# Kernel tuning notes

Hardware: AMD Instinct MI355X
Metric: run time of the kernel (lower is better)

Reference implementation:

```python
import jax, jax.numpy as jnp
import numpy as np

B, N, E, H = 64, 2048, 256, 256


def _scan_dir(xproj, Whh, bhh, reverse):
    # xproj: (B, N, H) precomputed input projection; recurrence h_t = tanh(xproj_t + h @ Whh.T + bhh)
    def step(h, xt):
        h = jnp.tanh(xt + h @ Whh.T + bhh)
        return h, h
    h0 = jnp.zeros((xproj.shape[0], Whh.shape[0]), xproj.dtype)
    _, seq = jax.lax.scan(step, h0, jnp.swapaxes(xproj, 0, 1), reverse=reverse)
    return jnp.swapaxes(seq, 0, 1)  # (B, N, H)


def _bilayer(inp, Wf, bf, Uf, cf, Wb, bb, Ub, cb):
    fore = _scan_dir(inp @ Wf.T + bf, Uf, cf, False)
    back = _scan_dir(inp @ Wb.T + bb, Ub, cb, True)
    return jnp.concatenate([fore, back], axis=-1), fore[:, -1, :], back[:, 0, :]


def setup_inputs() -> dict:
    key = jax.random.key(0)
    ks = jax.random.split(key, 17)
    s_e = 1.0 / np.sqrt(E)
    s_h = 1.0 / np.sqrt(H)
    s_2h = 1.0 / np.sqrt(2 * H)
    f32 = jnp.float32
    return {
        'x': jax.random.normal(ks[0], (B, N, E), f32),
        'Wih_f0': jax.random.normal(ks[1], (H, E), f32) * s_e,
        'bih_f0': jax.random.normal(ks[2], (H,), f32) * s_e,
        'Whh_f0': jax.random.normal(ks[3], (H, H), f32) * s_h,
        'bhh_f0': jax.random.normal(ks[4], (H,), f32) * s_h,
        'Wih_b0': jax.random.normal(ks[5], (H, E), f32) * s_e,
        'bih_b0': jax.random.normal(ks[6], (H,), f32) * s_e,
        'Whh_b0': jax.random.normal(ks[7], (H, H), f32) * s_h,
        'bhh_b0': jax.random.normal(ks[8], (H,), f32) * s_h,
        'Wih_f1': jax.random.normal(ks[9], (H, 2 * H), f32) * s_2h,
        'bih_f1': jax.random.normal(ks[10], (H,), f32) * s_2h,
        'Whh_f1': jax.random.normal(ks[11], (H, H), f32) * s_h,
        'bhh_f1': jax.random.normal(ks[12], (H,), f32) * s_h,
        'Wih_b1': jax.random.normal(ks[13], (H, 2 * H), f32) * s_2h,
        'bih_b1': jax.random.normal(ks[14], (H,), f32) * s_2h,
        'Whh_b1': jax.random.normal(ks[15], (H, H), f32) * s_h,
        'bhh_b1': jax.random.normal(ks[16], (H,), f32) * s_h,
    }


def reference(x, Wih_f0, bih_f0, Whh_f0, bhh_f0, Wih_b0, bih_b0, Whh_b0, bhh_b0,
              Wih_f1, bih_f1, Whh_f1, bhh_f1, Wih_b1, bih_b1, Whh_b1, bhh_b1):
    out0, _, _ = _bilayer(x, Wih_f0, bih_f0, Whh_f0, bhh_f0, Wih_b0, bih_b0, Whh_b0, bhh_b0)
    _, h_f, h_b = _bilayer(out0, Wih_f1, bih_f1, Whh_f1, bhh_f1, Wih_b1, bih_b1, Whh_b1, bhh_b1)
    return jnp.concatenate([h_f, h_b], axis=-1)  # (B, 2H) final hidden of last layer
```

## Files before the change

kernel.cpp:

```cpp
#include <hip/hip_runtime.h>

#define BATCH 64
#define SEQ   2048
#define EIN   256
#define HID   256

typedef _Float16 f16;
typedef _Float16 f16x8 __attribute__((ext_vector_type(8)));
typedef float    f32x4 __attribute__((ext_vector_type(4)));

__global__ __launch_bounds__(256) void cast_f32_f16(
    const float* __restrict__ s, f16* __restrict__ d, int n)
{
    int i = (blockIdx.x * 256 + threadIdx.x) * 8;
    if (i >= n) return;
    const float4* sp = reinterpret_cast<const float4*>(s + i);
    float4 a = sp[0], b = sp[1];
    f16x8 v = { (f16)a.x, (f16)a.y, (f16)a.z, (f16)a.w,
                (f16)b.x, (f16)b.y, (f16)b.z, (f16)b.w };
    *reinterpret_cast<f16x8*>(d + i) = v;
}

__global__ __launch_bounds__(256, 2) void gemm_proj(
    const f16* __restrict__ A, const f16* __restrict__ W,
    const float* __restrict__ bias, f16* __restrict__ C, int K)
{
    const int tid  = threadIdx.x;
    const int wave = tid >> 6, lane = tid & 63;
    const int g    = lane >> 4, lr = lane & 15;
    const int bm   = blockIdx.x * 128;
    const int bn   = blockIdx.y * 128;
    const int wm   = (wave >> 1) * 64, wn = (wave & 1) * 64;

    __shared__ __align__(16) f16 As[128][72];
    __shared__ __align__(16) f16 Bs[128][72];

    f32x4 acc[4][4] = {};

    for (int kt = 0; kt < K; kt += 64) {
        __syncthreads();
#pragma unroll
        for (int i = 0; i < 4; ++i) {
            int c = i * 256 + tid;
            int r = c >> 3, sg = c & 7;
            *reinterpret_cast<f16x8*>(&As[r][sg * 8]) =
                *reinterpret_cast<const f16x8*>(A + (size_t)(bm + r) * K + kt + sg * 8);
            *reinterpret_cast<f16x8*>(&Bs[r][sg * 8]) =
                *reinterpret_cast<const f16x8*>(W + (size_t)(bn + r) * K + kt + sg * 8);
        }
        __syncthreads();
#pragma unroll
        for (int kf = 0; kf < 2; ++kf) {
            f16x8 af[4], bf[4];
#pragma unroll
            for (int f = 0; f < 4; ++f) {
                af[f] = *reinterpret_cast<const f16x8*>(&As[wm + f * 16 + lr][kf * 32 + g * 8]);
                bf[f] = *reinterpret_cast<const f16x8*>(&Bs[wn + f * 16 + lr][kf * 32 + g * 8]);
            }
#pragma unroll
            for (int fm = 0; fm < 4; ++fm)
#pragma unroll
                for (int fn = 0; fn < 4; ++fn)
                    acc[fm][fn] = __builtin_amdgcn_mfma_f32_16x16x32_f16(
                        af[fm], bf[fn], acc[fm][fn], 0, 0, 0);
        }
    }

#pragma unroll
    for (int fn = 0; fn < 4; ++fn) {
        float bv = bias[bn + wn + fn * 16 + lr];
#pragma unroll
        for (int fm = 0; fm < 4; ++fm) {
#pragma unroll
            for (int i = 0; i < 4; ++i) {
                int row = bm + wm + fm * 16 + g * 4 + i;
                int col = bn + wn + fn * 16 + lr;
                C[(size_t)row * 256 + col] = (f16)(acc[fm][fn][i] + bv);
            }
        }
    }
}

template<bool WRITE_SEQ>
__global__ __launch_bounds__(256, 1) void rnn_scan(
    const f16* __restrict__ xpF, const f16* __restrict__ xpB,
    const float* __restrict__ WhhF, const float* __restrict__ bhhF,
    const float* __restrict__ WhhB, const float* __restrict__ bhhB,
    f16* __restrict__ seq_out,
    float* __restrict__ fin_out)
{
    const int blk = blockIdx.x;
    const int b   = blk >> 1, dir = blk & 1;
    const f16*   xp  = dir ? xpB : xpF;
    const float* Whh = dir ? WhhB : WhhF;
    const float* bhh = dir ? bhhB : bhhF;

    const int tid  = threadIdx.x;
    const int wave = tid >> 6, lane = tid & 63;
    const int g    = lane >> 4, lr = lane & 15;
    const int n0   = wave * 64;

    __shared__ __align__(16) f16 hbuf[2][256];

    f16x8 wf[4][8];
#pragma unroll
    for (int fn = 0; fn < 4; ++fn) {
        const float* wr = Whh + (size_t)(n0 + fn * 16 + lr) * 256;
#pragma unroll
        for (int kf = 0; kf < 8; ++kf) {
            const float4* p = reinterpret_cast<const float4*>(wr + kf * 32 + g * 8);
            float4 x0 = p[0], x1 = p[1];
            wf[fn][kf] = (f16x8){ (f16)x0.x, (f16)x0.y, (f16)x0.z, (f16)x0.w,
                                  (f16)x1.x, (f16)x1.y, (f16)x1.z, (f16)x1.w };
        }
    }
    const float bv = bhh[tid];

    hbuf[0][tid] = (f16)0.f;
    __syncthreads();

    const long long xstep = dir ? -256 : 256;
    const f16* xptr = xp + (long long)b * SEQ * 256 + (long long)(dir ? SEQ - 1 : 0) * 256 + tid;

    const long long sstep = dir ? -512 : 512;
    f16* sptr = nullptr;
    if (WRITE_SEQ)
        sptr = seq_out + ((long long)b * SEQ + (dir ? SEQ - 1 : 0)) * 512 + dir * 256 + tid;

    f16 ring[4];
#pragma unroll
    for (int r = 0; r < 3; ++r) ring[r] = xptr[(long long)r * xstep];
    const f16* xpre = xptr + 3 * xstep;

    const f32x4 zf = {0.f, 0.f, 0.f, 0.f};
    float last_h = 0.f;

    for (int s4 = 0; s4 < SEQ; s4 += 4) {
#pragma unroll
        for (int u = 0; u < 4; ++u) {
            const int rd = u & 1;

            f16x8 af[8];
#pragma unroll
            for (int kf = 0; kf < 8; ++kf)
                af[kf] = *reinterpret_cast<const f16x8*>(&hbuf[rd][kf * 32 + g * 8]);

            ring[(u + 3) & 3] = *xpre;
            xpre += xstep;

            f32x4 alo[4], ahi[4];
#pragma unroll
            for (int fn = 0; fn < 4; ++fn) {
                alo[fn] = __builtin_amdgcn_mfma_f32_16x16x32_f16(af[0], wf[fn][0], zf, 0, 0, 0);
                ahi[fn] = __builtin_amdgcn_mfma_f32_16x16x32_f16(af[4], wf[fn][4], zf, 0, 0, 0);
            }
#pragma unroll
            for (int kf = 1; kf < 4; ++kf)
#pragma unroll
                for (int fn = 0; fn < 4; ++fn) {
                    alo[fn] = __builtin_amdgcn_mfma_f32_16x16x32_f16(af[kf],     wf[fn][kf],     alo[fn], 0, 0, 0);
                    ahi[fn] = __builtin_amdgcn_mfma_f32_16x16x32_f16(af[kf + 4], wf[fn][kf + 4], ahi[fn], 0, 0, 0);
                }

            float lo01 = (g & 1) ? alo[1][0] : alo[0][0];
            float lo23 = (g & 1) ? alo[3][0] : alo[2][0];
            float lo   = (g & 2) ? lo23 : lo01;
            float hi01 = (g & 1) ? ahi[1][0] : ahi[0][0];
            float hi23 = (g & 1) ? ahi[3][0] : ahi[2][0];
            float hi   = (g & 2) ? hi23 : hi01;

            float pre = lo + hi + (float)ring[u & 3] + bv;
            float e  = __expf(pre + pre);
            float h  = 1.0f - 2.0f * __builtin_amdgcn_rcpf(e + 1.0f);
            f16 hh   = (f16)h;
            last_h   = h;

            hbuf[rd ^ 1][tid] = hh;

            if (WRITE_SEQ) {
                *sptr = hh;
                sptr += sstep;
            }

            asm volatile("s_waitcnt lgkmcnt(0)" ::: "memory");
            __builtin_amdgcn_s_barrier();
            asm volatile("" ::: "memory");
        }
    }

    if (!WRITE_SEQ)
        fin_out[b * 512 + dir * 256 + tid] = last_h;
}

extern "C" void kernel_launch(void* const* d_in, const int* in_sizes, int n_in,
                              void* d_out, int out_size, void* d_ws, size_t ws_size,
                              hipStream_t stream)
{
    (void)in_sizes; (void)n_in; (void)out_size; (void)ws_size;

    const float* x      = (const float*)d_in[0];
    const float* Wih_f0 = (const float*)d_in[1];
    const float* bih_f0 = (const float*)d_in[2];
    const float* Whh_f0 = (const float*)d_in[3];
    const float* bhh_f0 = (const float*)d_in[4];
    const float* Wih_b0 = (const float*)d_in[5];
    const float* bih_b0 = (const float*)d_in[6];
    const float* Whh_b0 = (const float*)d_in[7];
    const float* bhh_b0 = (const float*)d_in[8];
    const float* Wih_f1 = (const float*)d_in[9];
    const float* bih_f1 = (const float*)d_in[10];
    const float* Whh_f1 = (const float*)d_in[11];
    const float* bhh_f1 = (const float*)d_in[12];
    const float* Wih_b1 = (const float*)d_in[13];
    const float* bih_b1 = (const float*)d_in[14];
    const float* Whh_b1 = (const float*)d_in[15];
    const float* bhh_b1 = (const float*)d_in[16];

    float* out = (float*)d_out;
    char*  ws  = (char*)d_ws;

    f16* xpF  = (f16*)(ws);
    f16* xpB  = (f16*)(ws + 67108864);
    f16* out0 = (f16*)(ws + 134217728);
    f16* x16  = (f16*)(ws + 268435456);
    f16* wf0  = (f16*)(ws + 335544320);
    f16* wb0  = (f16*)(ws + 335544320 + 131072);
    f16* wf1  = (f16*)(ws + 335544320 + 262144);
    f16* wb1  = (f16*)(ws + 335544320 + 524288);

    cast_f32_f16<<<16384, 256, 0, stream>>>(x, x16, 33554432);
    cast_f32_f16<<<32,    256, 0, stream>>>(Wih_f0, wf0, 65536);
    cast_f32_f16<<<32,    256, 0, stream>>>(Wih_b0, wb0, 65536);
    cast_f32_f16<<<64,    256, 0, stream>>>(Wih_f1, wf1, 131072);
    cast_f32_f16<<<64,    256, 0, stream>>>(Wih_b1, wb1, 131072);

    gemm_proj<<<dim3(1024, 2), 256, 0, stream>>>(x16, wf0, bih_f0, xpF, 256);
    gemm_proj<<<dim3(1024, 2), 256, 0, stream>>>(x16, wb0, bih_b0, xpB, 256);

    rnn_scan<true><<<128, 256, 0, stream>>>(xpF, xpB, Whh_f0, bhh_f0, Whh_b0, bhh_b0,
                                            out0, nullptr);

    gemm_proj<<<dim3(1024, 2), 256, 0, stream>>>(out0, wf1, bih_f1, xpF, 512);
    gemm_proj<<<dim3(1024, 2), 256, 0, stream>>>(out0, wb1, bih_b1, xpB, 512);

    rnn_scan<false><<<128, 256, 0, stream>>>(xpF, xpB, Whh_f1, bhh_f1, Whh_b1, bhh_b1,
                                             nullptr, out);
}
```

Before: 1.910 ms.

## Rotate per-wave K order and prefetch own-wave hidden chunks before barrier

Each wave now walks the K dimension of the recurrent matmul in a rotated order that starts at the hidden slice it writes itself. It can then load those two A fragments from LDS right after its own writes land, before the block barrier, which takes part of the LDS read latency off the serial per-timestep critical path. The two 4-deep accumulator chains become one 8-deep chain per output tile, and tanh uses exp2 with a folded constant. The risk is longer MFMA dependency chains and slightly different fp accumulation order.

```diff
diff --git a/kernel.cpp b/kernel.cpp
--- a/kernel.cpp
+++ b/kernel.cpp
@@ -102,26 +102,40 @@
 
     __shared__ __align__(16) f16 hbuf[2][256];
 
+    int kfj[8];
+#pragma unroll
+    for (int j = 0; j < 8; ++j) kfj[j] = (2 * wave + j) & 7;
+
     f16x8 wf[4][8];
 #pragma unroll
     for (int fn = 0; fn < 4; ++fn) {
         const float* wr = Whh + (size_t)(n0 + fn * 16 + lr) * 256;
 #pragma unroll
-        for (int kf = 0; kf < 8; ++kf) {
-            const float4* p = reinterpret_cast<const float4*>(wr + kf * 32 + g * 8);
+        for (int j = 0; j < 8; ++j) {
+            const float4* p = reinterpret_cast<const float4*>(wr + kfj[j] * 32 + g * 8);
             float4 x0 = p[0], x1 = p[1];
-            wf[fn][kf] = (f16x8){ (f16)x0.x, (f16)x0.y, (f16)x0.z, (f16)x0.w,
-                                  (f16)x1.x, (f16)x1.y, (f16)x1.z, (f16)x1.w };
+            wf[fn][j] = (f16x8){ (f16)x0.x, (f16)x0.y, (f16)x0.z, (f16)x0.w,
+                                 (f16)x1.x, (f16)x1.y, (f16)x1.z, (f16)x1.w };
         }
     }
     const float bv = bhh[tid];
+
+    int aoff[8];
+#pragma unroll
+    for (int j = 0; j < 8; ++j) aoff[j] = kfj[j] * 64 + g * 16;
+    char* lds0 = (char*)&hbuf[0][0];
+    char* lds1 = (char*)&hbuf[1][0];
 
     hbuf[0][tid] = (f16)0.f;
     __syncthreads();
 
     const long long xstep = dir ? -256 : 256;
-    const f16* xptr = xp + (long long)b * SEQ * 256 + (long long)(dir ? SEQ - 1 : 0) * 256 + tid;
-
+    const f16* xpre;
+    {
+        const f16* xptr = xp + (long long)b * SEQ * 256
+                             + (long long)(dir ? SEQ - 1 : 0) * 256 + tid;
+        xpre = xptr;
+    }
     const long long sstep = dir ? -512 : 512;
     f16* sptr = nullptr;
     if (WRITE_SEQ)
@@ -129,53 +143,49 @@
 
     f16 ring[4];
 #pragma unroll
-    for (int r = 0; r < 3; ++r) ring[r] = xptr[(long long)r * xstep];
-    const f16* xpre = xptr + 3 * xstep;
+    for (int r = 0; r < 3; ++r) { ring[r] = *xpre; xpre += xstep; }
 
     const f32x4 zf = {0.f, 0.f, 0.f, 0.f};
     float last_h = 0.f;
 
+    f16x8 af[8];
+    af[0] = *reinterpret_cast<const f16x8*>(lds0 + aoff[0]);
+    af[1] = *reinterpret_cast<const f16x8*>(lds0 + aoff[1]);
+
     for (int s4 = 0; s4 < SEQ; s4 += 4) {
 #pragma unroll
         for (int u = 0; u < 4; ++u) {
-            const int rd = u & 1;
-
-            f16x8 af[8];
-#pragma unroll
-            for (int kf = 0; kf < 8; ++kf)
-                af[kf] = *reinterpret_cast<const f16x8*>(&hbuf[rd][kf * 32 + g * 8]);
+            char* cur = (u & 1) ? lds1 : lds0;
+            char* nxt = (u & 1) ? lds0 : lds1;
+
+#pragma unroll
+            for (int j = 2; j < 8; ++j)
+                af[j] = *reinterpret_cast<const f16x8*>(cur + aoff[j]);
 
             ring[(u + 3) & 3] = *xpre;
             xpre += xstep;
 
-            f32x4 alo[4], ahi[4];
-#pragma unroll
-            for (int fn = 0; fn < 4; ++fn) {
-                alo[fn] = __builtin_amdgcn_mfma_f32_16x16x32_f16(af[0], wf[fn][0], zf, 0, 0, 0);
-                ahi[fn] = __builtin_amdgcn_mfma_f32_16x16x32_f16(af[4], wf[fn][4], zf, 0, 0, 0);
-            }
-#pragma unroll
-            for (int kf = 1; kf < 4; ++kf)
-#pragma unroll
-                for (int fn = 0; fn < 4; ++fn) {
-                    alo[fn] = __builtin_amdgcn_mfma_f32_16x16x32_f16(af[kf],     wf[fn][kf],     alo[fn], 0, 0, 0);
-                    ahi[fn] = __builtin_amdgcn_mfma_f32_16x16x32_f16(af[kf + 4], wf[fn][kf + 4], ahi[fn], 0, 0, 0);
-                }
-
-            float lo01 = (g & 1) ? alo[1][0] : alo[0][0];
-            float lo23 = (g & 1) ? alo[3][0] : alo[2][0];
-            float lo   = (g & 2) ? lo23 : lo01;
-            float hi01 = (g & 1) ? ahi[1][0] : ahi[0][0];
-            float hi23 = (g & 1) ? ahi[3][0] : ahi[2][0];
-            float hi   = (g & 2) ? hi23 : hi01;
-
-            float pre = lo + hi + (float)ring[u & 3] + bv;
-            float e  = __expf(pre + pre);
+            f32x4 acc[4];
+#pragma unroll
+            for (int fn = 0; fn < 4; ++fn)
+                acc[fn] = __builtin_amdgcn_mfma_f32_16x16x32_f16(af[0], wf[fn][0], zf, 0, 0, 0);
+#pragma unroll
+            for (int j = 1; j < 8; ++j)
+#pragma unroll
+                for (int fn = 0; fn < 4; ++fn)
+                    acc[fn] = __builtin_amdgcn_mfma_f32_16x16x32_f16(af[j], wf[fn][j], acc[fn], 0, 0, 0);
+
+            float r01 = (g & 1) ? acc[1][0] : acc[0][0];
+            float r23 = (g & 1) ? acc[3][0] : acc[2][0];
+            float mv  = (g & 2) ? r23 : r01;
+
+            float pre = mv + (float)ring[u & 3] + bv;
+            float e  = __builtin_exp2f(pre * 2.885390082f);
             float h  = 1.0f - 2.0f * __builtin_amdgcn_rcpf(e + 1.0f);
             f16 hh   = (f16)h;
             last_h   = h;
 
-            hbuf[rd ^ 1][tid] = hh;
+            *reinterpret_cast<f16*>(nxt + tid * 2) = hh;
 
             if (WRITE_SEQ) {
                 *sptr = hh;
@@ -183,6 +193,9 @@
             }
 
             asm volatile("s_waitcnt lgkmcnt(0)" ::: "memory");
+            af[0] = *reinterpret_cast<const f16x8*>(nxt + aoff[0]);
+            af[1] = *reinterpret_cast<const f16x8*>(nxt + aoff[1]);
+
             __builtin_amdgcn_s_barrier();
             asm volatile("" ::: "memory");
         }
```

New measurement: 1.870 ms. 1.02x faster.

## Fuse x cast into projection GEMM and fold recurrent bias into projection

Applied to the files above, without the earlier changes.

The separate f32-to-f16 cast of the large input tensor is removed; the layer-0 projection GEMM now loads f32 directly and converts while staging into shared memory. The recurrent bias is added in the GEMM epilogue, which removes one add per step from the serial scan. The scan's split lo/hi MFMA accumulator chains are merged into a single chain, and tanh now uses exp2 with a prescaled argument. Merging the chains lengthens the dependent MFMA chain on the critical recurrence path, and the first projection GEMM now reads f32 input twice, once per direction.

```diff
diff --git a/kernel.cpp b/kernel.cpp
--- a/kernel.cpp
+++ b/kernel.cpp
@@ -21,9 +21,11 @@
     *reinterpret_cast<f16x8*>(d + i) = v;
 }
 
+template<typename AT>
 __global__ __launch_bounds__(256, 2) void gemm_proj(
-    const f16* __restrict__ A, const f16* __restrict__ W,
-    const float* __restrict__ bias, f16* __restrict__ C, int K)
+    const AT* __restrict__ A, const f16* __restrict__ W,
+    const float* __restrict__ bias_a, const float* __restrict__ bias_b,
+    f16* __restrict__ C, int K)
 {
     const int tid  = threadIdx.x;
     const int wave = tid >> 6, lane = tid & 63;
@@ -43,8 +45,17 @@
         for (int i = 0; i < 4; ++i) {
             int c = i * 256 + tid;
             int r = c >> 3, sg = c & 7;
-            *reinterpret_cast<f16x8*>(&As[r][sg * 8]) =
-                *reinterpret_cast<const f16x8*>(A + (size_t)(bm + r) * K + kt + sg * 8);
+            if constexpr (sizeof(AT) == 4) {
+                const float4* ap = reinterpret_cast<const float4*>(
+                    (const float*)A + (size_t)(bm + r) * K + kt + sg * 8);
+                float4 a0 = ap[0], a1 = ap[1];
+                f16x8 v = { (f16)a0.x, (f16)a0.y, (f16)a0.z, (f16)a0.w,
+                            (f16)a1.x, (f16)a1.y, (f16)a1.z, (f16)a1.w };
+                *reinterpret_cast<f16x8*>(&As[r][sg * 8]) = v;
+            } else {
+                *reinterpret_cast<f16x8*>(&As[r][sg * 8]) =
+                    *reinterpret_cast<const f16x8*>((const f16*)A + (size_t)(bm + r) * K + kt + sg * 8);
+            }
             *reinterpret_cast<f16x8*>(&Bs[r][sg * 8]) =
                 *reinterpret_cast<const f16x8*>(W + (size_t)(bn + r) * K + kt + sg * 8);
         }
@@ -68,13 +79,13 @@
 
 #pragma unroll
     for (int fn = 0; fn < 4; ++fn) {
-        float bv = bias[bn + wn + fn * 16 + lr];
+        int col = bn + wn + fn * 16 + lr;
+        float bv = bias_a[col] + bias_b[col];
 #pragma unroll
         for (int fm = 0; fm < 4; ++fm) {
 #pragma unroll
             for (int i = 0; i < 4; ++i) {
                 int row = bm + wm + fm * 16 + g * 4 + i;
-                int col = bn + wn + fn * 16 + lr;
                 C[(size_t)row * 256 + col] = (f16)(acc[fm][fn][i] + bv);
             }
         }
@@ -84,8 +95,7 @@
 template<bool WRITE_SEQ>
 __global__ __launch_bounds__(256, 1) void rnn_scan(
     const f16* __restrict__ xpF, const f16* __restrict__ xpB,
-    const float* __restrict__ WhhF, const float* __restrict__ bhhF,
-    const float* __restrict__ WhhB, const float* __restrict__ bhhB,
+    const float* __restrict__ WhhF, const float* __restrict__ WhhB,
     f16* __restrict__ seq_out,
     float* __restrict__ fin_out)
 {
@@ -93,7 +103,6 @@
     const int b   = blk >> 1, dir = blk & 1;
     const f16*   xp  = dir ? xpB : xpF;
     const float* Whh = dir ? WhhB : WhhF;
-    const float* bhh = dir ? bhhB : bhhF;
 
     const int tid  = threadIdx.x;
     const int wave = tid >> 6, lane = tid & 63;
@@ -114,14 +123,13 @@
                                   (f16)x1.x, (f16)x1.y, (f16)x1.z, (f16)x1.w };
         }
     }
-    const float bv = bhh[tid];
 
     hbuf[0][tid] = (f16)0.f;
     __syncthreads();
 
     const long long xstep = dir ? -256 : 256;
-    const f16* xptr = xp + (long long)b * SEQ * 256 + (long long)(dir ? SEQ - 1 : 0) * 256 + tid;
-
+    const f16* xpre = xp + (long long)b * SEQ * 256
+                         + (long long)(dir ? SEQ - 1 : 0) * 256 + tid;
     const long long sstep = dir ? -512 : 512;
     f16* sptr = nullptr;
     if (WRITE_SEQ)
@@ -129,8 +137,7 @@
 
     f16 ring[4];
 #pragma unroll
-    for (int r = 0; r < 3; ++r) ring[r] = xptr[(long long)r * xstep];
-    const f16* xpre = xptr + 3 * xstep;
+    for (int r = 0; r < 3; ++r) { ring[r] = *xpre; xpre += xstep; }
 
     const f32x4 zf = {0.f, 0.f, 0.f, 0.f};
     float last_h = 0.f;
@@ -148,29 +155,22 @@
             ring[(u + 3) & 3] = *xpre;
             xpre += xstep;
 
-            f32x4 alo[4], ahi[4];
-#pragma unroll
-            for (int fn = 0; fn < 4; ++fn) {
-                alo[fn] = __builtin_amdgcn_mfma_f32_16x16x32_f16(af[0], wf[fn][0], zf, 0, 0, 0);
-                ahi[fn] = __builtin_amdgcn_mfma_f32_16x16x32_f16(af[4], wf[fn][4], zf, 0, 0, 0);
-            }
-#pragma unroll
-            for (int kf = 1; kf < 4; ++kf)
-#pragma unroll
-                for (int fn = 0; fn < 4; ++fn) {
-                    alo[fn] = __builtin_amdgcn_mfma_f32_16x16x32_f16(af[kf],     wf[fn][kf],     alo[fn], 0, 0, 0);
-                    ahi[fn] = __builtin_amdgcn_mfma_f32_16x16x32_f16(af[kf + 4], wf[fn][kf + 4], ahi[fn], 0, 0, 0);
-                }
-
-            float lo01 = (g & 1) ? alo[1][0] : alo[0][0];
-            float lo23 = (g & 1) ? alo[3][0] : alo[2][0];
-            float lo   = (g & 2) ? lo23 : lo01;
-            float hi01 = (g & 1) ? ahi[1][0] : ahi[0][0];
-            float hi23 = (g & 1) ? ahi[3][0] : ahi[2][0];
-            float hi   = (g & 2) ? hi23 : hi01;
-
-            float pre = lo + hi + (float)ring[u & 3] + bv;
-            float e  = __expf(pre + pre);
+            f32x4 acc[4];
+#pragma unroll
+            for (int fn = 0; fn < 4; ++fn)
+                acc[fn] = __builtin_amdgcn_mfma_f32_16x16x32_f16(af[0], wf[fn][0], zf, 0, 0, 0);
+#pragma unroll
+            for (int kf = 1; kf < 8; ++kf)
+#pragma unroll
+                for (int fn = 0; fn < 4; ++fn)
+                    acc[fn] = __builtin_amdgcn_mfma_f32_16x16x32_f16(af[kf], wf[fn][kf], acc[fn], 0, 0, 0);
+
+            float r01 = (g & 1) ? acc[1][0] : acc[0][0];
+            float r23 = (g & 1) ? acc[3][0] : acc[2][0];
+            float mv  = (g & 2) ? r23 : r01;
+
+            float pre = mv + (float)ring[u & 3];
+            float e  = __builtin_exp2f(pre * 2.885390082f);
             float h  = 1.0f - 2.0f * __builtin_amdgcn_rcpf(e + 1.0f);
             f16 hh   = (f16)h;
             last_h   = h;
@@ -222,27 +222,23 @@
     f16* xpF  = (f16*)(ws);
     f16* xpB  = (f16*)(ws + 67108864);
     f16* out0 = (f16*)(ws + 134217728);
-    f16* x16  = (f16*)(ws + 268435456);
-    f16* wf0  = (f16*)(ws + 335544320);
-    f16* wb0  = (f16*)(ws + 335544320 + 131072);
-    f16* wf1  = (f16*)(ws + 335544320 + 262144);
-    f16* wb1  = (f16*)(ws + 335544320 + 524288);
-
-    cast_f32_f16<<<16384, 256, 0, stream>>>(x, x16, 33554432);
-    cast_f32_f16<<<32,    256, 0, stream>>>(Wih_f0, wf0, 65536);
-    cast_f32_f16<<<32,    256, 0, stream>>>(Wih_b0, wb0, 65536);
-    cast_f32_f16<<<64,    256, 0, stream>>>(Wih_f1, wf1, 131072);
-    cast_f32_f16<<<64,    256, 0, stream>>>(Wih_b1, wb1, 131072);
-
-    gemm_proj<<<dim3(1024, 2), 256, 0, stream>>>(x16, wf0, bih_f0, xpF, 256);
-    gemm_proj<<<dim3(1024, 2), 256, 0, stream>>>(x16, wb0, bih_b0, xpB, 256);
-
-    rnn_scan<true><<<128, 256, 0, stream>>>(xpF, xpB, Whh_f0, bhh_f0, Whh_b0, bhh_b0,
-                                            out0, nullptr);
-
-    gemm_proj<<<dim3(1024, 2), 256, 0, stream>>>(out0, wf1, bih_f1, xpF, 512);
-    gemm_proj<<<dim3(1024, 2), 256, 0, stream>>>(out0, wb1, bih_b1, xpB, 512);
-
-    rnn_scan<false><<<128, 256, 0, stream>>>(xpF, xpB, Whh_f1, bhh_f1, Whh_b1, bhh_b1,
-                                             nullptr, out);
-}
+    f16* wf0  = (f16*)(ws + 268435456);
+    f16* wb0  = (f16*)(ws + 268435456 + 131072);
+    f16* wf1  = (f16*)(ws + 268435456 + 262144);
+    f16* wb1  = (f16*)(ws + 268435456 + 524288);
+
+    cast_f32_f16<<<32, 256, 0, stream>>>(Wih_f0, wf0, 65536);
+    cast_f32_f16<<<32, 256, 0, stream>>>(Wih_b0, wb0, 65536);
+    cast_f32_f16<<<64, 256, 0, stream>>>(Wih_f1, wf1, 131072);
+    cast_f32_f16<<<64, 256, 0, stream>>>(Wih_b1, wb1, 131072);
+
+    gemm_proj<float><<<dim3(1024, 2), 256, 0, stream>>>(x, wf0, bih_f0, bhh_f0, xpF, 256);
+    gemm_proj<float><<<dim3(1024, 2), 256, 0, stream>>>(x, wb0, bih_b0, bhh_b0, xpB, 256);
+
+    rnn_scan<true><<<128, 256, 0, stream>>>(xpF, xpB, Whh_f0, Whh_b0, out0, nullptr);
+
+    gemm_proj<f16><<<dim3(1024, 2), 256, 0, stream>>>(out0, wf1, bih_f1, bhh_f1, xpF, 512);
+    gemm_proj<f16><<<dim3(1024, 2), 256, 0, stream>>>(out0, wb1, bih_b1, bhh_b1, xpB, 512);
+
+    rnn_scan<false><<<128, 256, 0, stream>>>(xpF, xpB, Whh_f1, Whh_b1, nullptr, out);
+}
```

Measured after the change: 2.171 ms. 13.7% more time.
